# Optimization experiments

Measured on AMD Instinct MI355X. Metric: run time of the kernel, lower is better.

## Reference

```python
import jax, jax.numpy as jnp
import numpy as np

B, D = 4096, 768

def setup_inputs() -> dict:
    key = jax.random.key(0)
    k1, k2 = jax.random.split(key)
    embeddings = jax.random.normal(k1, (B, D), dtype=jnp.float32)
    # precomputed articulatory distance matrix (stand-in for articulatory_distance_fn over word pairs)
    art_dist = jax.random.uniform(k2, (B, B), dtype=jnp.float32)
    return {"embeddings": embeddings, "art_dist": art_dist}

def reference(embeddings, art_dist):
    b = embeddings.shape[0]
    # pairwise squared L2 distances via Gram matrix: ||ei||^2 + ||ej||^2 - 2 ei.ej
    sq = jnp.sum(embeddings * embeddings, axis=1)                  # [B]
    gram = jnp.einsum('id,jd->ij', embeddings, embeddings)         # [B, B]
    d2 = sq[:, None] + sq[None, :] - 2.0 * gram                    # [B, B]
    off_diag = 1.0 - jnp.eye(b, dtype=embeddings.dtype)            # exclude i == j
    pair_loss = (d2 - art_dist) ** 2
    pairs_count = b * (b - 1)
    return jnp.sum(pair_loss * off_diag) / pairs_count
```

## Files before the change

### kernel.cpp

```cpp
#include <hip/hip_runtime.h>
#include <hip/hip_bf16.h>

#define B_DIM 4096
#define D_DIM 768
#define BM 128
#define BN 128
#define BK 64
#define NT (B_DIM / BM)

typedef __bf16 bf16_t;
typedef bf16_t bf16x8 __attribute__((ext_vector_type(8)));
typedef float f32x4 __attribute__((ext_vector_type(4)));

static __device__ __forceinline__ ushort f2bf(float v) {
    __hip_bfloat16 h = __float2bfloat16(v);
    return *reinterpret_cast<const ushort*>(&h);
}

__global__ __launch_bounds__(256) void prep_kernel(
    const float* __restrict__ E, ushort* __restrict__ Ebf, float* __restrict__ sq)
{
    const int lane = threadIdx.x & 63;
    const int row  = blockIdx.x * 4 + (threadIdx.x >> 6);
    const float4* er = reinterpret_cast<const float4*>(E + (size_t)row * D_DIM);
    ushort4* br = reinterpret_cast<ushort4*>(Ebf + (size_t)row * D_DIM);
    float s = 0.f;
    #pragma unroll
    for (int k = 0; k < 3; ++k) {
        float4 v = er[lane + 64 * k];
        s += v.x * v.x + v.y * v.y + v.z * v.z + v.w * v.w;
        ushort4 o;
        o.x = f2bf(v.x); o.y = f2bf(v.y); o.z = f2bf(v.z); o.w = f2bf(v.w);
        br[lane + 64 * k] = o;
    }
    #pragma unroll
    for (int off = 32; off > 0; off >>= 1) s += __shfl_down(s, off);
    if (lane == 0) sq[row] = s;
}

__global__ __launch_bounds__(256) void gram_loss_kernel(
    const ushort* __restrict__ Ebf, const float* __restrict__ sq,
    const float* __restrict__ art, float* __restrict__ out)
{
    __shared__ ushort Als[BM][BK];
    __shared__ ushort Bls[BN][BK];
    __shared__ float red[4];

    const int tid  = threadIdx.x;
    const int lane = tid & 63;
    const int wave = tid >> 6;
    const int wr = wave >> 1;
    const int wc = wave & 1;

    int b = blockIdx.x, I = 0, rem = NT;
    while (b >= rem) { b -= rem; ++I; --rem; }
    const int J = I + b;
    const int row0 = I * BM;
    const int col0 = J * BN;

    f32x4 acc[4][4] = {};

    const int srow  = tid >> 3;
    const int scol8 = (tid & 7) * 8;

    for (int kk = 0; kk < D_DIM; kk += BK) {
        #pragma unroll
        for (int i = 0; i < 4; ++i) {
            const int r = i * 32 + srow;
            const int colg = scol8 ^ ((r & 7) << 3);
            const ushort* gA = Ebf + (size_t)(row0 + r) * D_DIM + kk + colg;
            __builtin_amdgcn_global_load_lds(
                (const __attribute__((address_space(1))) void*)gA,
                (__attribute__((address_space(3))) void*)(&Als[r][scol8]),
                16, 0, 0);
            const ushort* gB = Ebf + (size_t)(col0 + r) * D_DIM + kk + colg;
            __builtin_amdgcn_global_load_lds(
                (const __attribute__((address_space(1))) void*)gB,
                (__attribute__((address_space(3))) void*)(&Bls[r][scol8]),
                16, 0, 0);
        }
        __syncthreads();

        #pragma unroll
        for (int k2 = 0; k2 < BK; k2 += 32) {
            bf16x8 af[4], bfr[4];
            #pragma unroll
            for (int m = 0; m < 4; ++m) {
                const int r = wr * 64 + m * 16 + (lane & 15);
                const int c = (k2 + (lane >> 4) * 8) ^ ((r & 7) << 3);
                af[m] = *reinterpret_cast<const bf16x8*>(&Als[r][c]);
            }
            #pragma unroll
            for (int n = 0; n < 4; ++n) {
                const int r = wc * 64 + n * 16 + (lane & 15);
                const int c = (k2 + (lane >> 4) * 8) ^ ((r & 7) << 3);
                bfr[n] = *reinterpret_cast<const bf16x8*>(&Bls[r][c]);
            }
            #pragma unroll
            for (int m = 0; m < 4; ++m)
                #pragma unroll
                for (int n = 0; n < 4; ++n)
                    acc[m][n] = __builtin_amdgcn_mfma_f32_16x16x32_bf16(
                        af[m], bfr[n], acc[m][n], 0, 0, 0);
        }
        __syncthreads();
    }

    float lsum = 0.f;
    const int lr = (lane >> 4) * 4;
    const int lc = lane & 15;
    const int rbase = row0 + wr * 64;
    const int cbase = col0 + wc * 64;

    if (I != J) {
        #pragma unroll
        for (int m = 0; m < 4; ++m) {
            const int gi0 = rbase + m * 16 + lr;
            #pragma unroll
            for (int n = 0; n < 4; ++n) {
                const int gj = cbase + n * 16 + lc;
                const float sqj = sq[gj];
                const float4 am = *reinterpret_cast<const float4*>(
                    &art[(size_t)gj * B_DIM + gi0]);
                const float amv[4] = { am.x, am.y, am.z, am.w };
                #pragma unroll
                for (int j = 0; j < 4; ++j) {
                    const int gi = gi0 + j;
                    const float d2 = sq[gi] + sqj - 2.0f * acc[m][n][j];
                    const float t1 = d2 - art[(size_t)gi * B_DIM + gj];
                    const float t2 = d2 - amv[j];
                    lsum += t1 * t1 + t2 * t2;
                }
            }
        }
    } else {
        #pragma unroll
        for (int m = 0; m < 4; ++m) {
            const int gi0 = rbase + m * 16 + lr;
            #pragma unroll
            for (int n = 0; n < 4; ++n) {
                const int gj = cbase + n * 16 + lc;
                const float sqj = sq[gj];
                #pragma unroll
                for (int j = 0; j < 4; ++j) {
                    const int gi = gi0 + j;
                    const float d2 = sq[gi] + sqj - 2.0f * acc[m][n][j];
                    const float t = d2 - art[(size_t)gi * B_DIM + gj];
                    if (gi != gj) lsum += t * t;
                }
            }
        }
    }

    #pragma unroll
    for (int off = 32; off > 0; off >>= 1) lsum += __shfl_down(lsum, off);
    if (lane == 0) red[wave] = lsum;
    __syncthreads();
    if (tid == 0) {
        const float inv_pairs = 1.0f / ((float)B_DIM * (float)(B_DIM - 1));
        atomicAdd(out, (red[0] + red[1] + red[2] + red[3]) * inv_pairs);
    }
}

extern "C" void kernel_launch(void* const* d_in, const int* in_sizes, int n_in,
                              void* d_out, int out_size, void* d_ws, size_t ws_size,
                              hipStream_t stream) {
    const float* E   = (const float*)d_in[0];
    const float* art = (const float*)d_in[1];
    float* out = (float*)d_out;

    ushort* Ebf = (ushort*)d_ws;
    float*  sq  = (float*)((char*)d_ws + (size_t)B_DIM * D_DIM * 2);

    hipMemsetAsync(d_out, 0, sizeof(float), stream);
    prep_kernel<<<B_DIM / 4, 256, 0, stream>>>(E, Ebf, sq);
    gram_loss_kernel<<<(NT * (NT + 1)) / 2, 256, 0, stream>>>(Ebf, sq, art, out);
}
```

Baseline: 151.3 us.

## Compute full Gram tile grid instead of exploiting symmetry, with swizzled block order

Replaces the upper-triangular tile schedule, which computed each off-diagonal tile once and read both art[i][j] and art[j][i], with a full 32x32 tile grid where each block reads only one art element per pair, through coalesced float4 loads of the transposed slice. Block indices are swizzled across groups of eight, presumably to spread neighbouring tiles across XCDs and caches. It also caches the row squared norms in registers and adds a min-blocks-per-CU launch bound. This roughly doubles the MFMA work in exchange for removing the strided scalar art loads and the triangular index loop.

Result: faster. 129.4 us (-14.5%).

```diff
diff --git a/kernel.cpp b/kernel.cpp
--- a/kernel.cpp
+++ b/kernel.cpp
@@ -38,7 +38,7 @@
     if (lane == 0) sq[row] = s;
 }
 
-__global__ __launch_bounds__(256) void gram_loss_kernel(
+__global__ __launch_bounds__(256, 4) void gram_loss_kernel(
     const ushort* __restrict__ Ebf, const float* __restrict__ sq,
     const float* __restrict__ art, float* __restrict__ out)
 {
@@ -52,11 +52,11 @@
     const int wr = wave >> 1;
     const int wc = wave & 1;
 
-    int b = blockIdx.x, I = 0, rem = NT;
-    while (b >= rem) { b -= rem; ++I; --rem; }
-    const int J = I + b;
-    const int row0 = I * BM;
-    const int col0 = J * BN;
+    const int swz = (blockIdx.x & 7) * 128 + (blockIdx.x >> 3);
+    const int tileR = swz >> 5;
+    const int tileC = swz & 31;
+    const int row0 = tileR * BM;
+    const int col0 = tileC * BN;
 
     f32x4 acc[4][4] = {};
 
@@ -112,10 +112,35 @@
     const int rbase = row0 + wr * 64;
     const int cbase = col0 + wc * 64;
 
-    if (I != J) {
+    if (tileR != tileC) {
         #pragma unroll
         for (int m = 0; m < 4; ++m) {
             const int gi0 = rbase + m * 16 + lr;
+            float sqi[4];
+            #pragma unroll
+            for (int j = 0; j < 4; ++j) sqi[j] = sq[gi0 + j];
+            #pragma unroll
+            for (int n = 0; n < 4; ++n) {
+                const int gj = cbase + n * 16 + lc;
+                const float sqj = sq[gj];
+                const float4 am = *reinterpret_cast<const float4*>(
+                    &art[(size_t)gj * B_DIM + gi0]);
+                const float amv[4] = { am.x, am.y, am.z, am.w };
+                #pragma unroll
+                for (int j = 0; j < 4; ++j) {
+                    const float d2 = sqi[j] + sqj - 2.0f * acc[m][n][j];
+                    const float t = d2 - amv[j];
+                    lsum += t * t;
+                }
+            }
+        }
+    } else {
+        #pragma unroll
+        for (int m = 0; m < 4; ++m) {
+            const int gi0 = rbase + m * 16 + lr;
+            float sqi[4];
+            #pragma unroll
+            for (int j = 0; j < 4; ++j) sqi[j] = sq[gi0 + j];
             #pragma unroll
             for (int n = 0; n < 4; ++n) {
                 const int gj = cbase + n * 16 + lc;
@@ -126,26 +151,8 @@
                 #pragma unroll
                 for (int j = 0; j < 4; ++j) {
                     const int gi = gi0 + j;
-                    const float d2 = sq[gi] + sqj - 2.0f * acc[m][n][j];
-                    const float t1 = d2 - art[(size_t)gi * B_DIM + gj];
-                    const float t2 = d2 - amv[j];
-                    lsum += t1 * t1 + t2 * t2;
-                }
-            }
-        }
-    } else {
-        #pragma unroll
-        for (int m = 0; m < 4; ++m) {
-            const int gi0 = rbase + m * 16 + lr;
-            #pragma unroll
-            for (int n = 0; n < 4; ++n) {
-                const int gj = cbase + n * 16 + lc;
-                const float sqj = sq[gj];
-                #pragma unroll
-                for (int j = 0; j < 4; ++j) {
-                    const int gi = gi0 + j;
-                    const float d2 = sq[gi] + sqj - 2.0f * acc[m][n][j];
-                    const float t = d2 - art[(size_t)gi * B_DIM + gj];
+                    const float d2 = sqi[j] + sqj - 2.0f * acc[m][n][j];
+                    const float t = d2 - amv[j];
                     if (gi != gj) lsum += t * t;
                 }
             }
@@ -174,5 +181,5 @@
 
     hipMemsetAsync(d_out, 0, sizeof(float), stream);
     prep_kernel<<<B_DIM / 4, 256, 0, stream>>>(E, Ebf, sq);
-    gram_loss_kernel<<<(NT * (NT + 1)) / 2, 256, 0, stream>>>(Ebf, sq, art, out);
+    gram_loss_kernel<<<NT * NT, 256, 0, stream>>>(Ebf, sq, art, out);
 }
```
